# Optimization experiments

Measured on AMD Instinct MI355X. Metric: run time of the kernel, lower is better.

The kernel has to match this reference:

```python
import jax, jax.numpy as jnp
import numpy as np

RANK = 2
ALPHA = 0.1
BASE_SCALE = 500.0
HIDDEN = 512
INPUT = 8
NUM_MIX = 2
NUM_SEEDS = 4
BATCH = 64
SEQ = 2048
D = 2 * RANK + INPUT  # 12


def setup_inputs() -> dict:
    key = jax.random.key(0)
    k1, k2, k3, k4 = jax.random.split(key, 4)
    x = jax.random.normal(k1, (BATCH, SEQ, INPUT), dtype=jnp.float32)
    means = jnp.zeros((NUM_MIX, D), dtype=jnp.float32)
    # mirror torch init: covariance (hence tril) scaled ~ 1/sqrt(hidden_size)
    scale_tril = jax.random.normal(k2, (NUM_MIX, D, D), dtype=jnp.float32) / jnp.sqrt(jnp.float32(HIDDEN))
    mixture_weights = jnp.ones((NUM_MIX,), dtype=jnp.float32)
    seeds = jax.random.normal(k3, (NUM_SEEDS, HIDDEN, D), dtype=jnp.float32)
    cur_seeds = jax.random.randint(k4, (BATCH,), 0, NUM_SEEDS, dtype=jnp.int32)
    return {"x": x, "means": means, "scale_tril": scale_tril,
            "mixture_weights": mixture_weights, "seeds": seeds, "cur_seeds": cur_seeds}


def _clamp_tril(scale_tril):
    # lower-triangular with strictly positive diagonal (matches _clamp_tril)
    diag = jnp.abs(jnp.diagonal(scale_tril, axis1=-2, axis2=-1) - 1e-12) + 1e-12
    return jnp.tril(scale_tril, -1) + jax.vmap(jnp.diag)(diag)


def reference(x, means, scale_tril, mixture_weights, seeds, cur_seeds):
    L = _clamp_tril(scale_tril)                       # (M, D, D)
    w = jnp.clip(mixture_weights, 1e-6, None)
    w = w / jnp.sum(w)                                # normalized mixture weights

    # samp[i, s, h, :] = means[i] + L[i] @ seeds[s, h]
    samp = jnp.einsum('ide,she->ishd', L, seeds) + means[:, None, None, :]
    comb = jnp.einsum('i,ishd->shd', w, samp)         # weighted mixture sum, (S, H, D)
    m = comb[..., :RANK]                              # (S, H, r)
    n = comb[..., RANK:2 * RANK]                      # (S, H, r)
    I = comb[..., 2 * RANK:]                          # (S, H, in)

    J = jnp.einsum('shr,sgr->shg', m, n) * (BASE_SCALE / HIDDEN)   # (S, H, H)

    Jb = J[cur_seeds]                                 # (B, H, H) per-sample recurrence matrix
    Ib = I[cur_seeds]                                 # (B, H, in)
    Ix = jnp.einsum('bhi,bti->bth', Ib, x)            # precomputed input injection (B, T, H)

    def step(h, ix_t):
        dh = -h + jnp.einsum('bhg,bg->bh', Jb, jnp.tanh(h)) + ix_t
        h = h + ALPHA * dh
        return h, h

    h0 = jnp.zeros((x.shape[0], HIDDEN), dtype=x.dtype)
    _, hiddens = jax.lax.scan(step, h0, jnp.swapaxes(Ix, 0, 1))    # (T, B, H)
    hiddens = jnp.swapaxes(hiddens, 0, 1)             # (B, T, H)

    # down_project=True: project onto span([m, I]) via pinv per seed
    span = jnp.concatenate([m, I], axis=-1)           # (S, H, r+in)
    pinv = jnp.linalg.pinv(span)                      # (S, r+in, H)
    out = jnp.einsum('bkh,bth->btk', pinv[cur_seeds], hiddens)     # (B, T, r+in)
    return out
```

## Files before the change

### kernel.cpp

```cpp
#include <hip/hip_runtime.h>
#include <math.h>

#define HIDDEN  512
#define INPUT   8
#define NUM_MIX 2
#define BATCH   64
#define SEQ     2048
#define DD      12
#define KOUT    10
#define TTILE   16
#define NTILES  (SEQ/TTILE)

#define SCALE_F 2.8853900817779268
#define AB_F    0.09765625f

typedef float v2f __attribute__((ext_vector_type(2)));
typedef float f4v __attribute__((ext_vector_type(4)));

__device__ __forceinline__ v2f pk_fma(v2f a, v2f b, v2f c) {
    return __builtin_elementwise_fma(a, b, c);
}

template<int CTRL>
__device__ __forceinline__ float dpp_add(float x) {
    int y = __builtin_amdgcn_update_dpp(0, __float_as_int(x), CTRL, 0xF, 0xF, true);
    return x + __int_as_float(y);
}
__device__ __forceinline__ float wave_allsum(float x) {
    x = dpp_add<0x111>(x);
    x = dpp_add<0x112>(x);
    x = dpp_add<0x114>(x);
    x = dpp_add<0x118>(x);
    x = dpp_add<0x142>(x);
    x = dpp_add<0x143>(x);
    return __int_as_float(__builtin_amdgcn_readlane(__float_as_int(x), 63));
}

__global__ __launch_bounds__(256) void fsm_rnn_kernel(
    const float* __restrict__ x,
    const float* __restrict__ means,
    const float* __restrict__ scale_tril,
    const float* __restrict__ mixw,
    const float* __restrict__ seeds,
    const int*   __restrict__ cur_seeds,
    float*       __restrict__ out)
{
    __shared__ __align__(16) float IxB[2][TTILE][HIDDEN];
    __shared__ __align__(16) float xsB[2][TTILE*INPUT];
    __shared__ __align__(16) float IvL[HIDDEN][INPUT];
    __shared__ float PM0[HIDDEN], PM1[HIDDEN], N0[HIDDEN], N1[HIDDEN];
    __shared__ __align__(8) float vring[2][TTILE][2];
    __shared__ double Leff[DD*DD];
    __shared__ double meansw[DD];

    const int tid  = threadIdx.x;
    const int lane = tid & 63;
    const int wid  = tid >> 6;
    const int b    = blockIdx.x;
    const int s    = cur_seeds[b];
    const float* xb = x + (size_t)b * SEQ * INPUT;
    float* outb = out + (size_t)b * SEQ * KOUT;

    double w0 = fmax((double)mixw[0], 1e-6);
    double w1 = fmax((double)mixw[1], 1e-6);
    double wsum = w0 + w1; w0 /= wsum; w1 /= wsum;

    if (tid < DD*DD) {
        int d = tid / DD, e = tid % DD;
        double acc = 0.0;
        #pragma unroll
        for (int i = 0; i < NUM_MIX; ++i) {
            float v = scale_tril[i*DD*DD + d*DD + e];
            float c = (d > e) ? v : (d == e ? fabsf(v - 1e-12f) + 1e-12f : 0.0f);
            acc += (i == 0 ? w0 : w1) * (double)c;
        }
        Leff[tid] = acc;
    }
    if (tid < DD)
        meansw[tid] = w0 * (double)means[tid] + w1 * (double)means[DD + tid];
    if (tid < 2*TTILE*INPUT)
        ((float*)xsB)[tid] = xb[tid];
    __syncthreads();

    #pragma unroll
    for (int rr = 0; rr < 2; ++rr) {
        int h = tid + rr*256;
        const float* sh = &seeds[(s*HIDDEN + h)*DD];
        double comb[DD];
        #pragma unroll
        for (int d = 0; d < DD; ++d) {
            double acc = meansw[d];
            for (int e = 0; e <= d; ++e)
                acc += Leff[d*DD + e] * (double)sh[e];
            comb[d] = acc;
        }
        PM0[h] = (float)(SCALE_F * (double)AB_F * comb[0]);
        PM1[h] = (float)(SCALE_F * (double)AB_F * comb[1]);
        N0[h]  = (float)comb[2];
        N1[h]  = (float)comb[3];
        #pragma unroll
        for (int i = 0; i < INPUT; ++i)
            IvL[h][i] = (float)(SCALE_F * 0.1 * comb[4 + i]);
    }
    __syncthreads();

    v2f AM0[4], AM1[4], NN0v[4], NN1v[4], H[4];
    f4v IvA[3], IvC[3];
    float zf = 0.0f, wst = 0.0f;
    const int pid = (wid - 1)*64 + lane;
    const int zi  = lane - 56;

    if (wid == 0) {
        #pragma unroll
        for (int q = 0; q < 4; ++q) {
            int ha = lane + 64*(2*q), hb = lane + 64*(2*q + 1);
            AM0[q]  = (v2f){PM0[ha], PM0[hb]};
            AM1[q]  = (v2f){PM1[ha], PM1[hb]};
            NN0v[q] = (v2f){N0[ha],  N0[hb]};
            NN1v[q] = (v2f){N1[ha],  N1[hb]};
            H[q]    = (v2f){0.0f, 0.0f};
        }
    } else {
        #pragma unroll
        for (int q = 0; q < 3; ++q) {
            int h = pid + 192*q;
            if (h < HIDDEN) {
                IvA[q] = *(const f4v*)&IvL[h][0];
                IvC[q] = *(const f4v*)&IvL[h][4];
            }
        }
    }

    auto produce = [&](int tg) {
        const int pb = tg & 1;
        const float* xs = xsB[pb];
        for (int tt = 0; tt < TTILE; ++tt) {
            f4v xa = *(const f4v*)&xs[tt*INPUT];
            f4v xc = *(const f4v*)&xs[tt*INPUT + 4];
            #pragma unroll
            for (int q = 0; q < 3; ++q) {
                int h = pid + 192*q;
                if (h < HIDDEN) {
                    float v =      IvA[q].x * xa.x;
                    v = fmaf(IvA[q].y, xa.y, v);
                    v = fmaf(IvA[q].z, xa.z, v);
                    v = fmaf(IvA[q].w, xa.w, v);
                    v = fmaf(IvC[q].x, xc.x, v);
                    v = fmaf(IvC[q].y, xc.y, v);
                    v = fmaf(IvC[q].z, xc.z, v);
                    v = fmaf(IvC[q].w, xc.w, v);
                    IxB[pb][tt][h] = v;
                }
            }
        }
        if (wid == 1 && lane >= 56) {
            #pragma unroll 4
            for (int tt = 0; tt < TTILE; ++tt) {
                zf = fmaf(0.9f, zf, 0.1f * xs[tt*INPUT + zi]);
                outb[(tg*TTILE + tt)*KOUT + 2 + zi] = zf;
            }
        }
    };

    auto process_w = [&](int tile) {
        if (lane == 54 || lane == 55) {
            const int widx = lane & 1;
            for (int tt = 0; tt < TTILE; ++tt) {
                wst = fmaf(0.9f, wst, AB_F * vring[tile & 1][tt][widx]);
                outb[(tile*TTILE + tt)*KOUT + widx] = wst;
            }
        }
    };

    if (wid != 0) produce(0);
    __syncthreads();

    for (int T = 0; T < NTILES; ++T) {
        if (wid == 0) {
            const int pb = T & 1;
            float cc[8], cn[8];
            #pragma unroll
            for (int j = 0; j < 8; ++j) cc[j] = IxB[pb][0][lane + 64*j];
            #pragma unroll
            for (int tt = 0; tt < TTILE; ++tt) {
                if (tt < TTILE-1) {
                    #pragma unroll
                    for (int j = 0; j < 8; ++j)
                        cn[j] = IxB[pb][tt+1][lane + 64*j];
                }
                v2f TH[4];
                #pragma unroll
                for (int q = 0; q < 4; ++q) {
                    v2f E;
                    E.x = __builtin_amdgcn_exp2f(H[q].x);
                    E.y = __builtin_amdgcn_exp2f(H[q].y);
                    v2f A = E + 1.0f;
                    v2f R;
                    R.x = __builtin_amdgcn_rcpf(A.x);
                    R.y = __builtin_amdgcn_rcpf(A.y);
                    const v2f m2 = {-2.0f, -2.0f}, one = {1.0f, 1.0f};
                    TH[q] = pk_fma(m2, R, one);
                }
                v2f s0 = TH[0]*NN0v[0];
                s0 = pk_fma(TH[1], NN0v[1], s0);
                s0 = pk_fma(TH[2], NN0v[2], s0);
                s0 = pk_fma(TH[3], NN0v[3], s0);
                v2f s1 = TH[0]*NN1v[0];
                s1 = pk_fma(TH[1], NN1v[1], s1);
                s1 = pk_fma(TH[2], NN1v[2], s1);
                s1 = pk_fma(TH[3], NN1v[3], s1);
                float p0 = s0.x + s0.y;
                float p1 = s1.x + s1.y;

                float v0 = wave_allsum(p0);
                float v1 = wave_allsum(p1);

                const v2f nine = {0.9f, 0.9f};
                v2f hc0 = pk_fma(nine, H[0], (v2f){cc[0], cc[1]});
                v2f hc1 = pk_fma(nine, H[1], (v2f){cc[2], cc[3]});
                v2f hc2 = pk_fma(nine, H[2], (v2f){cc[4], cc[5]});
                v2f hc3 = pk_fma(nine, H[3], (v2f){cc[6], cc[7]});

                v2f v0v = {v0, v0}, v1v = {v1, v1};
                H[0] = pk_fma(AM0[0], v0v, pk_fma(AM1[0], v1v, hc0));
                H[1] = pk_fma(AM0[1], v0v, pk_fma(AM1[1], v1v, hc1));
                H[2] = pk_fma(AM0[2], v0v, pk_fma(AM1[2], v1v, hc2));
                H[3] = pk_fma(AM0[3], v0v, pk_fma(AM1[3], v1v, hc3));

                if (lane == 0)
                    *(v2f*)&vring[pb][tt][0] = (v2f){v0, v1};

                #pragma unroll
                for (int j = 0; j < 8; ++j) cc[j] = cn[j];
            }
        } else {
            if (T + 1 < NTILES) produce(T + 1);
            if (wid == 2 && T + 2 < NTILES) {
                const int base = (T + 2)*(TTILE*INPUT);
                xsB[T & 1][lane]      = xb[base + lane];
                xsB[T & 1][lane + 64] = xb[base + lane + 64];
            }
            if (wid == 1 && T >= 1) process_w(T - 1);
        }
        __syncthreads();
    }
    if (wid == 1) process_w(NTILES - 1);
}

extern "C" void kernel_launch(void* const* d_in, const int* in_sizes, int n_in,
                              void* d_out, int out_size, void* d_ws, size_t ws_size,
                              hipStream_t stream) {
    (void)d_ws; (void)ws_size;
    const float* x          = (const float*)d_in[0];
    const float* means      = (const float*)d_in[1];
    const float* scale_tril = (const float*)d_in[2];
    const float* mixw       = (const float*)d_in[3];
    const float* seeds      = (const float*)d_in[4];
    const int*   cur_seeds  = (const int*)d_in[5];
    float* out = (float*)d_out;

    fsm_rnn_kernel<<<BATCH, 256, 0, stream>>>(
        x, means, scale_tril, mixw, seeds, cur_seeds, out);
}
```

Measured before the change: 519.8 us.

## Process two batch sequences per block to interleave independent recurrences

Each block now handles two batch elements, and the single recurrence wave advances both hidden states in the same step. The aim is to hide the latency of the serial exp/rcp and cross-lane reduction chain by interleaving two independent dependency chains. Shared memory is unioned so the setup buffers and the doubled Ix buffers fit. Only 32 blocks are launched, so fewer CUs are used, and each step does twice the work on one wave.

```diff
diff --git a/kernel.cpp b/kernel.cpp
--- a/kernel.cpp
+++ b/kernel.cpp
@@ -45,21 +45,27 @@
     const int*   __restrict__ cur_seeds,
     float*       __restrict__ out)
 {
-    __shared__ __align__(16) float IxB[2][TTILE][HIDDEN];
-    __shared__ __align__(16) float xsB[2][TTILE*INPUT];
-    __shared__ __align__(16) float IvL[HIDDEN][INPUT];
-    __shared__ float PM0[HIDDEN], PM1[HIDDEN], N0[HIDDEN], N1[HIDDEN];
-    __shared__ __align__(8) float vring[2][TTILE][2];
+    __shared__ union {
+        struct {
+            float IvL[2][HIDDEN][INPUT];
+            float PM[2][4][HIDDEN];
+        } s;
+        float IxB[2][2][TTILE][HIDDEN];
+    } u;
+    __shared__ __align__(16) float xsB[2][2][TTILE*INPUT];
+    __shared__ __align__(8)  float vring[2][2][TTILE][2];
     __shared__ double Leff[DD*DD];
     __shared__ double meansw[DD];
 
     const int tid  = threadIdx.x;
     const int lane = tid & 63;
     const int wid  = tid >> 6;
-    const int b    = blockIdx.x;
-    const int s    = cur_seeds[b];
-    const float* xb = x + (size_t)b * SEQ * INPUT;
-    float* outb = out + (size_t)b * SEQ * KOUT;
+    const int g    = blockIdx.x;
+    const float* xb[2]   = { x   + (size_t)(2*g  )*SEQ*INPUT,
+                             x   + (size_t)(2*g+1)*SEQ*INPUT };
+    float*       outb[2] = { out + (size_t)(2*g  )*SEQ*KOUT,
+                             out + (size_t)(2*g+1)*SEQ*KOUT };
+    const int sd[2] = { cur_seeds[2*g], cur_seeds[2*g+1] };
 
     double w0 = fmax((double)mixw[0], 1e-6);
     double w1 = fmax((double)mixw[1], 1e-6);
@@ -78,96 +84,111 @@
     }
     if (tid < DD)
         meansw[tid] = w0 * (double)means[tid] + w1 * (double)means[DD + tid];
-    if (tid < 2*TTILE*INPUT)
-        ((float*)xsB)[tid] = xb[tid];
+    ((float*)xsB)[tid]       = xb[0][tid];
+    ((float*)xsB)[256 + tid] = xb[1][tid];
     __syncthreads();
 
     #pragma unroll
-    for (int rr = 0; rr < 2; ++rr) {
-        int h = tid + rr*256;
-        const float* sh = &seeds[(s*HIDDEN + h)*DD];
-        double comb[DD];
-        #pragma unroll
-        for (int d = 0; d < DD; ++d) {
-            double acc = meansw[d];
-            for (int e = 0; e <= d; ++e)
-                acc += Leff[d*DD + e] * (double)sh[e];
-            comb[d] = acc;
-        }
-        PM0[h] = (float)(SCALE_F * (double)AB_F * comb[0]);
-        PM1[h] = (float)(SCALE_F * (double)AB_F * comb[1]);
-        N0[h]  = (float)comb[2];
-        N1[h]  = (float)comb[3];
-        #pragma unroll
-        for (int i = 0; i < INPUT; ++i)
-            IvL[h][i] = (float)(SCALE_F * 0.1 * comb[4 + i]);
+    for (int bi = 0; bi < 2; ++bi) {
+        #pragma unroll
+        for (int rr = 0; rr < 2; ++rr) {
+            int h = tid + rr*256;
+            const float* sh = &seeds[(sd[bi]*HIDDEN + h)*DD];
+            double comb[DD];
+            #pragma unroll
+            for (int d = 0; d < DD; ++d) {
+                double acc = meansw[d];
+                for (int e = 0; e <= d; ++e)
+                    acc += Leff[d*DD + e] * (double)sh[e];
+                comb[d] = acc;
+            }
+            u.s.PM[bi][0][h] = (float)(SCALE_F * (double)AB_F * comb[0]);
+            u.s.PM[bi][1][h] = (float)(SCALE_F * (double)AB_F * comb[1]);
+            u.s.PM[bi][2][h] = (float)comb[2];
+            u.s.PM[bi][3][h] = (float)comb[3];
+            #pragma unroll
+            for (int i = 0; i < INPUT; ++i)
+                u.s.IvL[bi][h][i] = (float)(SCALE_F * 0.1 * comb[4 + i]);
+        }
     }
     __syncthreads();
 
-    v2f AM0[4], AM1[4], NN0v[4], NN1v[4], H[4];
-    f4v IvA[3], IvC[3];
+    v2f AM0[2][4], AM1[2][4], NN0[2][4], NN1[2][4], H[2][4];
+    f4v IvA[2][3], IvC[2][3];
     float zf = 0.0f, wst = 0.0f;
     const int pid = (wid - 1)*64 + lane;
     const int zi  = lane - 56;
 
     if (wid == 0) {
         #pragma unroll
-        for (int q = 0; q < 4; ++q) {
-            int ha = lane + 64*(2*q), hb = lane + 64*(2*q + 1);
-            AM0[q]  = (v2f){PM0[ha], PM0[hb]};
-            AM1[q]  = (v2f){PM1[ha], PM1[hb]};
-            NN0v[q] = (v2f){N0[ha],  N0[hb]};
-            NN1v[q] = (v2f){N1[ha],  N1[hb]};
-            H[q]    = (v2f){0.0f, 0.0f};
+        for (int bi = 0; bi < 2; ++bi) {
+            #pragma unroll
+            for (int q = 0; q < 4; ++q) {
+                int ha = lane + 64*(2*q), hb = lane + 64*(2*q + 1);
+                AM0[bi][q] = (v2f){u.s.PM[bi][0][ha], u.s.PM[bi][0][hb]};
+                AM1[bi][q] = (v2f){u.s.PM[bi][1][ha], u.s.PM[bi][1][hb]};
+                NN0[bi][q] = (v2f){u.s.PM[bi][2][ha], u.s.PM[bi][2][hb]};
+                NN1[bi][q] = (v2f){u.s.PM[bi][3][ha], u.s.PM[bi][3][hb]};
+                H[bi][q]   = (v2f){0.0f, 0.0f};
+            }
         }
     } else {
         #pragma unroll
-        for (int q = 0; q < 3; ++q) {
-            int h = pid + 192*q;
-            if (h < HIDDEN) {
-                IvA[q] = *(const f4v*)&IvL[h][0];
-                IvC[q] = *(const f4v*)&IvL[h][4];
-            }
-        }
-    }
-
-    auto produce = [&](int tg) {
-        const int pb = tg & 1;
-        const float* xs = xsB[pb];
-        for (int tt = 0; tt < TTILE; ++tt) {
-            f4v xa = *(const f4v*)&xs[tt*INPUT];
-            f4v xc = *(const f4v*)&xs[tt*INPUT + 4];
+        for (int bi = 0; bi < 2; ++bi) {
             #pragma unroll
             for (int q = 0; q < 3; ++q) {
                 int h = pid + 192*q;
                 if (h < HIDDEN) {
-                    float v =      IvA[q].x * xa.x;
-                    v = fmaf(IvA[q].y, xa.y, v);
-                    v = fmaf(IvA[q].z, xa.z, v);
-                    v = fmaf(IvA[q].w, xa.w, v);
-                    v = fmaf(IvC[q].x, xc.x, v);
-                    v = fmaf(IvC[q].y, xc.y, v);
-                    v = fmaf(IvC[q].z, xc.z, v);
-                    v = fmaf(IvC[q].w, xc.w, v);
-                    IxB[pb][tt][h] = v;
-                }
-            }
-        }
-        if (wid == 1 && lane >= 56) {
+                    IvA[bi][q] = *(const f4v*)&u.s.IvL[bi][h][0];
+                    IvC[bi][q] = *(const f4v*)&u.s.IvL[bi][h][4];
+                }
+            }
+        }
+    }
+    __syncthreads();
+
+    auto produce = [&](int tg) {
+        const int pb = tg & 1;
+        #pragma unroll
+        for (int bi = 0; bi < 2; ++bi) {
+            const float* xs = xsB[bi][pb];
+            for (int tt = 0; tt < TTILE; ++tt) {
+                f4v xa = *(const f4v*)&xs[tt*INPUT];
+                f4v xc = *(const f4v*)&xs[tt*INPUT + 4];
+                #pragma unroll
+                for (int q = 0; q < 3; ++q) {
+                    int h = pid + 192*q;
+                    if (h < HIDDEN) {
+                        float v =      IvA[bi][q].x * xa.x;
+                        v = fmaf(IvA[bi][q].y, xa.y, v);
+                        v = fmaf(IvA[bi][q].z, xa.z, v);
+                        v = fmaf(IvA[bi][q].w, xa.w, v);
+                        v = fmaf(IvC[bi][q].x, xc.x, v);
+                        v = fmaf(IvC[bi][q].y, xc.y, v);
+                        v = fmaf(IvC[bi][q].z, xc.z, v);
+                        v = fmaf(IvC[bi][q].w, xc.w, v);
+                        u.IxB[bi][pb][tt][h] = v;
+                    }
+                }
+            }
+        }
+        if ((wid == 1 || wid == 2) && lane >= 56) {
+            const int bi = wid - 1;
+            const float* xs = xsB[bi][pb];
             #pragma unroll 4
             for (int tt = 0; tt < TTILE; ++tt) {
                 zf = fmaf(0.9f, zf, 0.1f * xs[tt*INPUT + zi]);
-                outb[(tg*TTILE + tt)*KOUT + 2 + zi] = zf;
+                outb[bi][(tg*TTILE + tt)*KOUT + 2 + zi] = zf;
             }
         }
     };
 
     auto process_w = [&](int tile) {
-        if (lane == 54 || lane == 55) {
-            const int widx = lane & 1;
+        if ((wid == 1 || wid == 2) && (lane == 54 || lane == 55)) {
+            const int bi = wid - 1, widx = lane & 1;
             for (int tt = 0; tt < TTILE; ++tt) {
-                wst = fmaf(0.9f, wst, AB_F * vring[tile & 1][tt][widx]);
-                outb[(tile*TTILE + tt)*KOUT + widx] = wst;
+                wst = fmaf(0.9f, wst, AB_F * vring[bi][tile & 1][tt][widx]);
+                outb[bi][(tile*TTILE + tt)*KOUT + widx] = wst;
             }
         }
     };
@@ -178,73 +199,95 @@
     for (int T = 0; T < NTILES; ++T) {
         if (wid == 0) {
             const int pb = T & 1;
-            float cc[8], cn[8];
-            #pragma unroll
-            for (int j = 0; j < 8; ++j) cc[j] = IxB[pb][0][lane + 64*j];
+            float cc[2][8], cn[2][8];
+            #pragma unroll
+            for (int j = 0; j < 8; ++j) {
+                cc[0][j] = u.IxB[0][pb][0][lane + 64*j];
+                cc[1][j] = u.IxB[1][pb][0][lane + 64*j];
+            }
             #pragma unroll
             for (int tt = 0; tt < TTILE; ++tt) {
                 if (tt < TTILE-1) {
                     #pragma unroll
-                    for (int j = 0; j < 8; ++j)
-                        cn[j] = IxB[pb][tt+1][lane + 64*j];
-                }
-                v2f TH[4];
-                #pragma unroll
-                for (int q = 0; q < 4; ++q) {
-                    v2f E;
-                    E.x = __builtin_amdgcn_exp2f(H[q].x);
-                    E.y = __builtin_amdgcn_exp2f(H[q].y);
-                    v2f A = E + 1.0f;
-                    v2f R;
-                    R.x = __builtin_amdgcn_rcpf(A.x);
-                    R.y = __builtin_amdgcn_rcpf(A.y);
-                    const v2f m2 = {-2.0f, -2.0f}, one = {1.0f, 1.0f};
-                    TH[q] = pk_fma(m2, R, one);
-                }
-                v2f s0 = TH[0]*NN0v[0];
-                s0 = pk_fma(TH[1], NN0v[1], s0);
-                s0 = pk_fma(TH[2], NN0v[2], s0);
-                s0 = pk_fma(TH[3], NN0v[3], s0);
-                v2f s1 = TH[0]*NN1v[0];
-                s1 = pk_fma(TH[1], NN1v[1], s1);
-                s1 = pk_fma(TH[2], NN1v[2], s1);
-                s1 = pk_fma(TH[3], NN1v[3], s1);
-                float p0 = s0.x + s0.y;
-                float p1 = s1.x + s1.y;
-
-                float v0 = wave_allsum(p0);
-                float v1 = wave_allsum(p1);
+                    for (int j = 0; j < 8; ++j) {
+                        cn[0][j] = u.IxB[0][pb][tt+1][lane + 64*j];
+                        cn[1][j] = u.IxB[1][pb][tt+1][lane + 64*j];
+                    }
+                }
+                v2f TH[2][4];
+                #pragma unroll
+                for (int bi = 0; bi < 2; ++bi) {
+                    #pragma unroll
+                    for (int q = 0; q < 4; ++q) {
+                        v2f E;
+                        E.x = __builtin_amdgcn_exp2f(H[bi][q].x);
+                        E.y = __builtin_amdgcn_exp2f(H[bi][q].y);
+                        v2f A = E + 1.0f;
+                        v2f R;
+                        R.x = __builtin_amdgcn_rcpf(A.x);
+                        R.y = __builtin_amdgcn_rcpf(A.y);
+                        const v2f m2 = {-2.0f, -2.0f}, one = {1.0f, 1.0f};
+                        TH[bi][q] = pk_fma(m2, R, one);
+                    }
+                }
+                float p0[2], p1[2];
+                #pragma unroll
+                for (int bi = 0; bi < 2; ++bi) {
+                    v2f s0 = TH[bi][0]*NN0[bi][0];
+                    s0 = pk_fma(TH[bi][1], NN0[bi][1], s0);
+                    s0 = pk_fma(TH[bi][2], NN0[bi][2], s0);
+                    s0 = pk_fma(TH[bi][3], NN0[bi][3], s0);
+                    v2f s1 = TH[bi][0]*NN1[bi][0];
+                    s1 = pk_fma(TH[bi][1], NN1[bi][1], s1);
+                    s1 = pk_fma(TH[bi][2], NN1[bi][2], s1);
+                    s1 = pk_fma(TH[bi][3], NN1[bi][3], s1);
+                    p0[bi] = s0.x + s0.y;
+                    p1[bi] = s1.x + s1.y;
+                }
+                float v0A = wave_allsum(p0[0]);
+                float v1A = wave_allsum(p1[0]);
+                float v0B = wave_allsum(p0[1]);
+                float v1B = wave_allsum(p1[1]);
 
                 const v2f nine = {0.9f, 0.9f};
-                v2f hc0 = pk_fma(nine, H[0], (v2f){cc[0], cc[1]});
-                v2f hc1 = pk_fma(nine, H[1], (v2f){cc[2], cc[3]});
-                v2f hc2 = pk_fma(nine, H[2], (v2f){cc[4], cc[5]});
-                v2f hc3 = pk_fma(nine, H[3], (v2f){cc[6], cc[7]});
-
-                v2f v0v = {v0, v0}, v1v = {v1, v1};
-                H[0] = pk_fma(AM0[0], v0v, pk_fma(AM1[0], v1v, hc0));
-                H[1] = pk_fma(AM0[1], v0v, pk_fma(AM1[1], v1v, hc1));
-                H[2] = pk_fma(AM0[2], v0v, pk_fma(AM1[2], v1v, hc2));
-                H[3] = pk_fma(AM0[3], v0v, pk_fma(AM1[3], v1v, hc3));
-
-                if (lane == 0)
-                    *(v2f*)&vring[pb][tt][0] = (v2f){v0, v1};
-
-                #pragma unroll
-                for (int j = 0; j < 8; ++j) cc[j] = cn[j];
+                float v0s[2] = {v0A, v0B}, v1s[2] = {v1A, v1B};
+                #pragma unroll
+                for (int bi = 0; bi < 2; ++bi) {
+                    v2f hc0 = pk_fma(nine, H[bi][0], (v2f){cc[bi][0], cc[bi][1]});
+                    v2f hc1 = pk_fma(nine, H[bi][1], (v2f){cc[bi][2], cc[bi][3]});
+                    v2f hc2 = pk_fma(nine, H[bi][2], (v2f){cc[bi][4], cc[bi][5]});
+                    v2f hc3 = pk_fma(nine, H[bi][3], (v2f){cc[bi][6], cc[bi][7]});
+                    v2f v0v = {v0s[bi], v0s[bi]}, v1v = {v1s[bi], v1s[bi]};
+                    H[bi][0] = pk_fma(AM0[bi][0], v0v, pk_fma(AM1[bi][0], v1v, hc0));
+                    H[bi][1] = pk_fma(AM0[bi][1], v0v, pk_fma(AM1[bi][1], v1v, hc1));
+                    H[bi][2] = pk_fma(AM0[bi][2], v0v, pk_fma(AM1[bi][2], v1v, hc2));
+                    H[bi][3] = pk_fma(AM0[bi][3], v0v, pk_fma(AM1[bi][3], v1v, hc3));
+                }
+                if (lane == 0) {
+                    *(v2f*)&vring[0][pb][tt][0] = (v2f){v0A, v1A};
+                    *(v2f*)&vring[1][pb][tt][0] = (v2f){v0B, v1B};
+                }
+                #pragma unroll
+                for (int j = 0; j < 8; ++j) {
+                    cc[0][j] = cn[0][j];
+                    cc[1][j] = cn[1][j];
+                }
             }
         } else {
             if (T + 1 < NTILES) produce(T + 1);
-            if (wid == 2 && T + 2 < NTILES) {
+            if (wid == 3 && T + 2 < NTILES) {
                 const int base = (T + 2)*(TTILE*INPUT);
-                xsB[T & 1][lane]      = xb[base + lane];
-                xsB[T & 1][lane + 64] = xb[base + lane + 64];
-            }
-            if (wid == 1 && T >= 1) process_w(T - 1);
+                #pragma unroll
+                for (int bi = 0; bi < 2; ++bi) {
+                    xsB[bi][T & 1][lane]      = xb[bi][base + lane];
+                    xsB[bi][T & 1][lane + 64] = xb[bi][base + lane + 64];
+                }
+            }
+            if (T >= 1) process_w(T - 1);
         }
         __syncthreads();
     }
-    if (wid == 1) process_w(NTILES - 1);
+    process_w(NTILES - 1);
 }
 
 extern "C" void kernel_launch(void* const* d_in, const int* in_sizes, int n_in,
@@ -259,6 +302,6 @@
     const int*   cur_seeds  = (const int*)d_in[5];
     float* out = (float*)d_out;
 
-    fsm_rnn_kernel<<<BATCH, 256, 0, stream>>>(
+    fsm_rnn_kernel<<<BATCH/2, 256, 0, stream>>>(
         x, means, scale_tril, mixw, seeds, cur_seeds, out);
 }
```

Result: slower. 914.5 us (+75.9%).
